# Performance work log

Hardware: AMD Instinct MI355X
Metric: run time of the kernel (lower is better)

The kernel has to match this reference:

```python
import jax, jax.numpy as jnp
import numpy as np

N_NODES = 20000
N_EDGES = 320000


def gcn_conv(x, W, b, src, dst, n_nodes):
    """PyG GCNConv: add self-loops, symmetric D^-1/2 (A+I) D^-1/2 normalization,
    linear transform then normalized scatter-add aggregation, plus bias."""
    x = x @ W  # [N, out]
    loop = jnp.arange(n_nodes, dtype=src.dtype)
    s = jnp.concatenate([src, loop])  # [E+N]
    d = jnp.concatenate([dst, loop])
    # degree of destination nodes (edge weight = 1), including self-loops
    deg = jax.ops.segment_sum(jnp.ones_like(d, dtype=x.dtype), d, num_segments=n_nodes)
    dinv = jnp.where(deg > 0, jax.lax.rsqrt(deg), 0.0)
    norm = dinv[s] * dinv[d]  # [E+N]
    msg = x[s] * norm[:, None]  # gather + scale, [E+N, out]
    out = jax.ops.segment_sum(msg, d, num_segments=n_nodes)  # scatter-add
    return out + b


def setup_inputs() -> dict:
    key = jax.random.key(0)
    ks = jax.random.split(key, 8)
    x = jax.random.normal(ks[0], (N_NODES, 10), dtype=jnp.float32)
    edge_index = jax.random.randint(ks[1], (2, N_EDGES), 0, N_NODES, dtype=jnp.int32)
    # Glorot-ish init for weights, zero bias (as in PyG defaults)
    def glorot(k, shape):
        lim = float(np.sqrt(6.0 / (shape[0] + shape[1])))
        return jax.random.uniform(k, shape, jnp.float32, -lim, lim)
    return {
        "x": x,
        "edge_index": edge_index,
        "W1": glorot(ks[2], (10, 256)),
        "b1": jnp.zeros((256,), jnp.float32),
        "W2": glorot(ks[3], (256, 128)),
        "b2": jnp.zeros((128,), jnp.float32),
        "W3": glorot(ks[4], (128, 1)),
        "b3": jnp.zeros((1,), jnp.float32),
    }


def reference(x, edge_index, W1, b1, W2, b2, W3, b3):
    src, dst = edge_index[0], edge_index[1]
    n = x.shape[0]
    h = jax.nn.relu(gcn_conv(x, W1, b1, src, dst, n))
    h = jax.nn.relu(gcn_conv(h, W2, b2, src, dst, n))
    out = gcn_conv(h, W3, b3, src, dst, n)
    return out.squeeze(-1)  # [N]
```

## Files before the change

kernel.cpp:

```cpp
#include <hip/hip_runtime.h>


constexpr int NN  = 20000;
constexpr int NE  = 320000;
constexpr int F0  = 10;
constexpr int F1  = 256;
constexpr int F2  = 128;
constexpr int MB  = 16;
constexpr int CAP = 64;


__global__ void k_fill(const int* __restrict__ src, const int* __restrict__ dst,
                       int* cursor, int* __restrict__ col) {
  int e = blockIdx.x * 256 + threadIdx.x;
  if (e >= NE) return;
  const int d = dst[e], s = src[e];
  const int pos = atomicAdd(&cursor[d], 1) & (CAP - 1);
  col[d * CAP + pos] = s;
}


__global__ __launch_bounds__(256) void k_gemm12(
    const float* __restrict__ x, const int* __restrict__ cursor,
    const int* __restrict__ col, const float* __restrict__ W1,
    const float* __restrict__ b1, const float* __restrict__ W2,
    float* __restrict__ t2s) {
  __shared__ float alds[MB * F0];
  __shared__ float h1[MB][F1 + 4];
  __shared__ float w2lds[32 * F2];
  const int tid = threadIdx.x;
  const int n0 = blockIdx.x * MB;
  {
    const int m = tid >> 4;
    const int f = tid & 15;
    if (f < F0) {
      const int n = n0 + m;
      const int deg = cursor[n];
      const int base = n * CAP;
      const float di = rsqrtf((float)(deg + 1));
      float acc = x[n * F0 + f] * di;
      int k = 0;
      for (; k + 3 < deg; k += 4) {
        const int s0 = col[base + k],     s1 = col[base + k + 1];
        const int s2 = col[base + k + 2], s3 = col[base + k + 3];
        const float d0 = rsqrtf((float)(cursor[s0] + 1));
        const float d1 = rsqrtf((float)(cursor[s1] + 1));
        const float d2 = rsqrtf((float)(cursor[s2] + 1));
        const float d3 = rsqrtf((float)(cursor[s3] + 1));
        acc += x[s0 * F0 + f] * d0 + x[s1 * F0 + f] * d1 +
               x[s2 * F0 + f] * d2 + x[s3 * F0 + f] * d3;
      }
      for (; k < deg; ++k) {
        const int s = col[base + k];
        acc += x[s * F0 + f] * rsqrtf((float)(cursor[s] + 1));
      }
      alds[m * F0 + f] = di * acc;
    }
  }
  float4 pf0 = *((const float4*)W2 + tid);
  float4 pf1 = *((const float4*)W2 + tid + 256);
  float4 pf2 = *((const float4*)W2 + tid + 512);
  float4 pf3 = *((const float4*)W2 + tid + 768);
  __syncthreads();
  {
    const int c = tid;
    float w1r[F0];
#pragma unroll
    for (int k = 0; k < F0; ++k) w1r[k] = W1[k * F1 + c];
    const float bb = b1[c];
#pragma unroll
    for (int m = 0; m < MB; ++m) {
      float acc = bb;
#pragma unroll
      for (int k = 0; k < F0; ++k) acc += alds[m * F0 + k] * w1r[k];
      h1[m][c] = fmaxf(acc, 0.f);
    }
  }
  const int cg_ = tid & 31;
  const int m0 = (tid >> 5) * 2;
  float a00 = 0.f, a01 = 0.f, a02 = 0.f, a03 = 0.f;
  float a10 = 0.f, a11 = 0.f, a12 = 0.f, a13 = 0.f;
#define FMA4(av, bv, vw)                                            \
  a00 += (av) * (vw).x; a01 += (av) * (vw).y;                       \
  a02 += (av) * (vw).z; a03 += (av) * (vw).w;                       \
  a10 += (bv) * (vw).x; a11 += (bv) * (vw).y;                       \
  a12 += (bv) * (vw).z; a13 += (bv) * (vw).w;
  for (int kc = 0; kc < F1 / 32; ++kc) {
    __syncthreads();
    {
      float4* ldst = (float4*)w2lds;
      ldst[tid] = pf0;
      ldst[tid + 256] = pf1;
      ldst[tid + 512] = pf2;
      ldst[tid + 768] = pf3;
    }
    __syncthreads();
    if (kc + 1 < F1 / 32) {
      const float4* gnext = (const float4*)(W2 + (kc + 1) * 32 * F2);
      pf0 = gnext[tid];
      pf1 = gnext[tid + 256];
      pf2 = gnext[tid + 512];
      pf3 = gnext[tid + 768];
    }
#pragma unroll
    for (int kk = 0; kk < 32; kk += 4) {
      const int k = kc * 32 + kk;
      const float4 ha = *(const float4*)&h1[m0][k];
      const float4 hb = *(const float4*)&h1[m0 + 1][k];
      const float4 w0 = *(const float4*)&w2lds[(kk + 0) * F2 + cg_ * 4];
      const float4 w1v = *(const float4*)&w2lds[(kk + 1) * F2 + cg_ * 4];
      const float4 w2v = *(const float4*)&w2lds[(kk + 2) * F2 + cg_ * 4];
      const float4 w3v = *(const float4*)&w2lds[(kk + 3) * F2 + cg_ * 4];
      FMA4(ha.x, hb.x, w0);
      FMA4(ha.y, hb.y, w1v);
      FMA4(ha.z, hb.z, w2v);
      FMA4(ha.w, hb.w, w3v);
    }
  }
#undef FMA4
  const float d0 = rsqrtf((float)(cursor[n0 + m0] + 1));
  const float d1 = rsqrtf((float)(cursor[n0 + m0 + 1] + 1));
  *(float4*)&t2s[(size_t)(n0 + m0) * F2 + cg_ * 4] =
      make_float4(a00 * d0, a01 * d0, a02 * d0, a03 * d0);
  *(float4*)&t2s[(size_t)(n0 + m0 + 1) * F2 + cg_ * 4] =
      make_float4(a10 * d1, a11 * d1, a12 * d1, a13 * d1);
}


__global__ __launch_bounds__(256) void k_agg2(
    const float* __restrict__ t2s, const int* __restrict__ cursor,
    const int* __restrict__ col, const float* __restrict__ b2,
    const float* __restrict__ W3, float* __restrict__ t3s) {
  const int wave = (blockIdx.x * 256 + threadIdx.x) >> 6;
  const int lane = threadIdx.x & 63;
  const int half = lane >> 5;
  const int li   = lane & 31;
  const int n    = wave * 2 + half;
  if (n >= NN) return;
  const int deg = cursor[n];
  const int base = n * CAP;
  const int fx = li * 4;
  const float4 vs = *(const float4*)&t2s[(size_t)n * F2 + fx];
  float a0 = vs.x, a1 = vs.y, a2 = vs.z, a3 = vs.w;
  int k = 0;
  for (; k + 7 < deg; k += 8) {
    const int s0 = col[base + k],     s1 = col[base + k + 1];
    const int s2 = col[base + k + 2], s3 = col[base + k + 3];
    const int s4 = col[base + k + 4], s5 = col[base + k + 5];
    const int s6 = col[base + k + 6], s7 = col[base + k + 7];
    const float4 v0 = *(const float4*)&t2s[(size_t)s0 * F2 + fx];
    const float4 v1 = *(const float4*)&t2s[(size_t)s1 * F2 + fx];
    const float4 v2 = *(const float4*)&t2s[(size_t)s2 * F2 + fx];
    const float4 v3 = *(const float4*)&t2s[(size_t)s3 * F2 + fx];
    const float4 v4 = *(const float4*)&t2s[(size_t)s4 * F2 + fx];
    const float4 v5 = *(const float4*)&t2s[(size_t)s5 * F2 + fx];
    const float4 v6 = *(const float4*)&t2s[(size_t)s6 * F2 + fx];
    const float4 v7 = *(const float4*)&t2s[(size_t)s7 * F2 + fx];
    a0 += ((v0.x + v1.x) + (v2.x + v3.x)) + ((v4.x + v5.x) + (v6.x + v7.x));
    a1 += ((v0.y + v1.y) + (v2.y + v3.y)) + ((v4.y + v5.y) + (v6.y + v7.y));
    a2 += ((v0.z + v1.z) + (v2.z + v3.z)) + ((v4.z + v5.z) + (v6.z + v7.z));
    a3 += ((v0.w + v1.w) + (v2.w + v3.w)) + ((v4.w + v5.w) + (v6.w + v7.w));
  }
  for (; k + 3 < deg; k += 4) {
    const int s0 = col[base + k],     s1 = col[base + k + 1];
    const int s2 = col[base + k + 2], s3 = col[base + k + 3];
    const float4 v0 = *(const float4*)&t2s[(size_t)s0 * F2 + fx];
    const float4 v1 = *(const float4*)&t2s[(size_t)s1 * F2 + fx];
    const float4 v2 = *(const float4*)&t2s[(size_t)s2 * F2 + fx];
    const float4 v3 = *(const float4*)&t2s[(size_t)s3 * F2 + fx];
    a0 += (v0.x + v1.x) + (v2.x + v3.x);
    a1 += (v0.y + v1.y) + (v2.y + v3.y);
    a2 += (v0.z + v1.z) + (v2.z + v3.z);
    a3 += (v0.w + v1.w) + (v2.w + v3.w);
  }
  for (; k < deg; ++k) {
    const float4 v = *(const float4*)&t2s[(size_t)col[base + k] * F2 + fx];
    a0 += v.x; a1 += v.y; a2 += v.z; a3 += v.w;
  }
  const float di = rsqrtf((float)(deg + 1));
  const float4 bb = *(const float4*)&b2[fx];
  const float4 w3 = *(const float4*)&W3[fx];
  const float h0 = fmaxf(di * a0 + bb.x, 0.f);
  const float h1 = fmaxf(di * a1 + bb.y, 0.f);
  const float h2 = fmaxf(di * a2 + bb.z, 0.f);
  const float h3 = fmaxf(di * a3 + bb.w, 0.f);
  float p = (h0 * w3.x + h1 * w3.y) + (h2 * w3.z + h3 * w3.w);
#pragma unroll
  for (int off = 16; off > 0; off >>= 1) p += __shfl_down(p, off);
  if (li == 0) t3s[n] = di * p;
}


__global__ void k_agg3(const float* __restrict__ t3s, const int* __restrict__ cursor,
                       const int* __restrict__ col, const float* __restrict__ b3,
                       float* __restrict__ out) {
  int n = blockIdx.x * 256 + threadIdx.x;
  if (n >= NN) return;
  const int deg = cursor[n];
  const int base = n * CAP;
  float acc = t3s[n];
  int k = 0;
  for (; k + 7 < deg; k += 8)
    acc += ((t3s[col[base + k]] + t3s[col[base + k + 1]]) +
            (t3s[col[base + k + 2]] + t3s[col[base + k + 3]])) +
           ((t3s[col[base + k + 4]] + t3s[col[base + k + 5]]) +
            (t3s[col[base + k + 6]] + t3s[col[base + k + 7]]));
  for (; k < deg; ++k) acc += t3s[col[base + k]];
  out[n] = rsqrtf((float)(deg + 1)) * acc + b3[0];
}

extern "C" void kernel_launch(void* const* d_in, const int* in_sizes, int n_in,
                              void* d_out, int out_size, void* d_ws, size_t ws_size,
                              hipStream_t stream) {
  const float* x = (const float*)d_in[0];
  const int* ei = (const int*)d_in[1];
  const int* srcv = ei;
  const int* dstv = ei + NE;
  const float* W1 = (const float*)d_in[2];
  const float* b1 = (const float*)d_in[3];
  const float* W2 = (const float*)d_in[4];
  const float* b2 = (const float*)d_in[5];
  const float* W3 = (const float*)d_in[6];
  const float* b3 = (const float*)d_in[7];
  float* out = (float*)d_out;

  char* w = (char*)d_ws;
  auto alloc = [&](size_t bytes) -> void* {
    void* p = (void*)w;
    w += (bytes + 255) & ~(size_t)255;
    return p;
  };
  int*   cursor = (int*)  alloc(NN * 4);
  int*   col    = (int*)  alloc((size_t)NN * CAP * 4);
  float* t2s    = (float*)alloc((size_t)NN * F2 * 4);
  float* t3s    = (float*)alloc(NN * 4);

  (void)hipMemsetAsync(cursor, 0, NN * 4, stream);
  k_fill<<<(NE + 255) / 256, 256, 0, stream>>>(srcv, dstv, cursor, col);
  k_gemm12<<<NN / MB, 256, 0, stream>>>(x, cursor, col, W1, b1, W2, t2s);
  k_agg2<<<NN / 8, 256, 0, stream>>>(t2s, cursor, col, b2, W3, t3s);
  k_agg3<<<(NN + 255) / 256, 256, 0, stream>>>(t3s, cursor, col, b3, out);
}
```

Baseline: 149.5 us.

## Double row tile in fused layer-1/GEMM2 kernel with 4x4 register blocking

The fused layer-1 aggregation plus W2 GEMM kernel now handles 32 nodes per block instead of 16, so each staged W2 tile is reused across twice as many rows. Each thread computes a 4x4 output block, and the first-layer aggregation is reorganised so all 256 threads cover features 0-7 and a 64-thread tail covers features 8-9. The aggregated features are stored with a padded stride so the W1 step can use float4 shared-memory loads. The costs are fewer blocks (625) for parallelism, more registers and LDS per block, and a serialized tail pass for the last two features.

```diff
diff --git a/kernel.cpp b/kernel.cpp
--- a/kernel.cpp
+++ b/kernel.cpp
@@ -6,8 +6,9 @@
 constexpr int F0  = 10;
 constexpr int F1  = 256;
 constexpr int F2  = 128;
-constexpr int MB  = 16;
+constexpr int MB  = 32;
 constexpr int CAP = 64;
+constexpr int AP  = 12;
 
 
 __global__ void k_fill(const int* __restrict__ src, const int* __restrict__ dst,
@@ -25,37 +26,60 @@
     const int* __restrict__ col, const float* __restrict__ W1,
     const float* __restrict__ b1, const float* __restrict__ W2,
     float* __restrict__ t2s) {
-  __shared__ float alds[MB * F0];
+  __shared__ float alds[MB * AP];
   __shared__ float h1[MB][F1 + 4];
   __shared__ float w2lds[32 * F2];
   const int tid = threadIdx.x;
   const int n0 = blockIdx.x * MB;
   {
-    const int m = tid >> 4;
-    const int f = tid & 15;
-    if (f < F0) {
-      const int n = n0 + m;
-      const int deg = cursor[n];
-      const int base = n * CAP;
-      const float di = rsqrtf((float)(deg + 1));
-      float acc = x[n * F0 + f] * di;
-      int k = 0;
-      for (; k + 3 < deg; k += 4) {
-        const int s0 = col[base + k],     s1 = col[base + k + 1];
-        const int s2 = col[base + k + 2], s3 = col[base + k + 3];
-        const float d0 = rsqrtf((float)(cursor[s0] + 1));
-        const float d1 = rsqrtf((float)(cursor[s1] + 1));
-        const float d2 = rsqrtf((float)(cursor[s2] + 1));
-        const float d3 = rsqrtf((float)(cursor[s3] + 1));
-        acc += x[s0 * F0 + f] * d0 + x[s1 * F0 + f] * d1 +
-               x[s2 * F0 + f] * d2 + x[s3 * F0 + f] * d3;
-      }
-      for (; k < deg; ++k) {
-        const int s = col[base + k];
-        acc += x[s * F0 + f] * rsqrtf((float)(cursor[s] + 1));
-      }
-      alds[m * F0 + f] = di * acc;
-    }
+    const int m = tid >> 3;
+    const int f = tid & 7;
+    const int n = n0 + m;
+    const int deg = cursor[n];
+    const int base = n * CAP;
+    const float di = rsqrtf((float)(deg + 1));
+    float acc = x[n * F0 + f] * di;
+    int k = 0;
+    for (; k + 3 < deg; k += 4) {
+      const int s0 = col[base + k],     s1 = col[base + k + 1];
+      const int s2 = col[base + k + 2], s3 = col[base + k + 3];
+      const float d0 = rsqrtf((float)(cursor[s0] + 1));
+      const float d1 = rsqrtf((float)(cursor[s1] + 1));
+      const float d2 = rsqrtf((float)(cursor[s2] + 1));
+      const float d3 = rsqrtf((float)(cursor[s3] + 1));
+      acc += x[s0 * F0 + f] * d0 + x[s1 * F0 + f] * d1 +
+             x[s2 * F0 + f] * d2 + x[s3 * F0 + f] * d3;
+    }
+    for (; k < deg; ++k) {
+      const int s = col[base + k];
+      acc += x[s * F0 + f] * rsqrtf((float)(cursor[s] + 1));
+    }
+    alds[m * AP + f] = di * acc;
+  }
+  if (tid < 64) {
+    const int m = tid >> 1;
+    const int f = 8 + (tid & 1);
+    const int n = n0 + m;
+    const int deg = cursor[n];
+    const int base = n * CAP;
+    const float di = rsqrtf((float)(deg + 1));
+    float acc = x[n * F0 + f] * di;
+    int k = 0;
+    for (; k + 3 < deg; k += 4) {
+      const int s0 = col[base + k],     s1 = col[base + k + 1];
+      const int s2 = col[base + k + 2], s3 = col[base + k + 3];
+      const float d0 = rsqrtf((float)(cursor[s0] + 1));
+      const float d1 = rsqrtf((float)(cursor[s1] + 1));
+      const float d2 = rsqrtf((float)(cursor[s2] + 1));
+      const float d3 = rsqrtf((float)(cursor[s3] + 1));
+      acc += x[s0 * F0 + f] * d0 + x[s1 * F0 + f] * d1 +
+             x[s2 * F0 + f] * d2 + x[s3 * F0 + f] * d3;
+    }
+    for (; k < deg; ++k) {
+      const int s = col[base + k];
+      acc += x[s * F0 + f] * rsqrtf((float)(cursor[s] + 1));
+    }
+    alds[m * AP + f] = di * acc;
   }
   float4 pf0 = *((const float4*)W2 + tid);
   float4 pf1 = *((const float4*)W2 + tid + 256);
@@ -70,21 +94,23 @@
     const float bb = b1[c];
 #pragma unroll
     for (int m = 0; m < MB; ++m) {
+      const float4 r0 = *(const float4*)&alds[m * AP + 0];
+      const float4 r1 = *(const float4*)&alds[m * AP + 4];
+      const float4 r2 = *(const float4*)&alds[m * AP + 8];
       float acc = bb;
-#pragma unroll
-      for (int k = 0; k < F0; ++k) acc += alds[m * F0 + k] * w1r[k];
+      acc += r0.x * w1r[0] + r0.y * w1r[1] + r0.z * w1r[2] + r0.w * w1r[3];
+      acc += r1.x * w1r[4] + r1.y * w1r[5] + r1.z * w1r[6] + r1.w * w1r[7];
+      acc += r2.x * w1r[8] + r2.y * w1r[9];
       h1[m][c] = fmaxf(acc, 0.f);
     }
   }
   const int cg_ = tid & 31;
-  const int m0 = (tid >> 5) * 2;
-  float a00 = 0.f, a01 = 0.f, a02 = 0.f, a03 = 0.f;
-  float a10 = 0.f, a11 = 0.f, a12 = 0.f, a13 = 0.f;
-#define FMA4(av, bv, vw)                                            \
-  a00 += (av) * (vw).x; a01 += (av) * (vw).y;                       \
-  a02 += (av) * (vw).z; a03 += (av) * (vw).w;                       \
-  a10 += (bv) * (vw).x; a11 += (bv) * (vw).y;                       \
-  a12 += (bv) * (vw).z; a13 += (bv) * (vw).w;
+  const int m0 = (tid >> 5) * 4;
+  float a[4][4] = {{0.f, 0.f, 0.f, 0.f}, {0.f, 0.f, 0.f, 0.f},
+                   {0.f, 0.f, 0.f, 0.f}, {0.f, 0.f, 0.f, 0.f}};
+#define FMA1(i, hv, vw4)                                            \
+  a[i][0] += (hv) * (vw4).x; a[i][1] += (hv) * (vw4).y;             \
+  a[i][2] += (hv) * (vw4).z; a[i][3] += (hv) * (vw4).w;
   for (int kc = 0; kc < F1 / 32; ++kc) {
     __syncthreads();
     {
@@ -105,25 +131,28 @@
 #pragma unroll
     for (int kk = 0; kk < 32; kk += 4) {
       const int k = kc * 32 + kk;
-      const float4 ha = *(const float4*)&h1[m0][k];
-      const float4 hb = *(const float4*)&h1[m0 + 1][k];
       const float4 w0 = *(const float4*)&w2lds[(kk + 0) * F2 + cg_ * 4];
       const float4 w1v = *(const float4*)&w2lds[(kk + 1) * F2 + cg_ * 4];
       const float4 w2v = *(const float4*)&w2lds[(kk + 2) * F2 + cg_ * 4];
       const float4 w3v = *(const float4*)&w2lds[(kk + 3) * F2 + cg_ * 4];
-      FMA4(ha.x, hb.x, w0);
-      FMA4(ha.y, hb.y, w1v);
-      FMA4(ha.z, hb.z, w2v);
-      FMA4(ha.w, hb.w, w3v);
-    }
-  }
-#undef FMA4
-  const float d0 = rsqrtf((float)(cursor[n0 + m0] + 1));
-  const float d1 = rsqrtf((float)(cursor[n0 + m0 + 1] + 1));
-  *(float4*)&t2s[(size_t)(n0 + m0) * F2 + cg_ * 4] =
-      make_float4(a00 * d0, a01 * d0, a02 * d0, a03 * d0);
-  *(float4*)&t2s[(size_t)(n0 + m0 + 1) * F2 + cg_ * 4] =
-      make_float4(a10 * d1, a11 * d1, a12 * d1, a13 * d1);
+      const float4 h0 = *(const float4*)&h1[m0 + 0][k];
+      const float4 hA = *(const float4*)&h1[m0 + 1][k];
+      const float4 hB = *(const float4*)&h1[m0 + 2][k];
+      const float4 hC = *(const float4*)&h1[m0 + 3][k];
+      FMA1(0, h0.x, w0); FMA1(0, h0.y, w1v); FMA1(0, h0.z, w2v); FMA1(0, h0.w, w3v);
+      FMA1(1, hA.x, w0); FMA1(1, hA.y, w1v); FMA1(1, hA.z, w2v); FMA1(1, hA.w, w3v);
+      FMA1(2, hB.x, w0); FMA1(2, hB.y, w1v); FMA1(2, hB.z, w2v); FMA1(2, hB.w, w3v);
+      FMA1(3, hC.x, w0); FMA1(3, hC.y, w1v); FMA1(3, hC.z, w2v); FMA1(3, hC.w, w3v);
+    }
+  }
+#undef FMA1
+#pragma unroll
+  for (int i = 0; i < 4; ++i) {
+    const int n = n0 + m0 + i;
+    const float dd = rsqrtf((float)(cursor[n] + 1));
+    *(float4*)&t2s[(size_t)n * F2 + cg_ * 4] =
+        make_float4(a[i][0] * dd, a[i][1] * dd, a[i][2] * dd, a[i][3] * dd);
+  }
 }
 
 
```

After: 151.9 us. Within noise of the previous version (+1.6%).
